# Kernel tuning notes

Measured on AMD Instinct MI355X. Metric: run time of the kernel, lower is better.

## Reference

```python
import jax, jax.numpy as jnp
import numpy as np

N = 32768
D = 512          # query_dim = key_dim = value_dim
H = 8            # num_heads


def setup_inputs() -> dict:
    key = jax.random.key(0)
    ks = jax.random.split(key, 8)
    s = 0.02
    return {
        "queries": jax.random.normal(ks[0], (N, D), dtype=jnp.float32),
        "keys": jax.random.normal(ks[1], (N, D), dtype=jnp.float32),
        "values": jax.random.normal(ks[2], (N, D), dtype=jnp.float32),
        # Linear weights stored as [in, out] (torch stores [out, in]; math identical)
        "Wq": jax.random.normal(ks[3], (D, D * H), dtype=jnp.float32) * s,
        "Wk": jax.random.normal(ks[4], (D, D * H), dtype=jnp.float32) * s,
        "Wv": jax.random.normal(ks[5], (D, D * H), dtype=jnp.float32) * s,
        "Wo": jax.random.normal(ks[6], (D * H, D), dtype=jnp.float32) * s,
        "bo": jax.random.normal(ks[7], (D,), dtype=jnp.float32) * s,
    }


def reference(queries, keys, values, Wq, Wk, Wv, Wo, bo):
    # Projections: [N, D] -> [N, H, D]
    Q = (queries @ Wq).reshape(-1, H, D)
    K = (keys @ Wk).reshape(-1, H, D)
    V = (values @ Wv).reshape(-1, H, D)
    # Per-token attention across the HEADS axis (faithful to torch.bmm on [N,H,D])
    attn = jnp.einsum("nhd,ngd->nhg", Q, K)      # [N, H, H], no 1/sqrt(d) scaling
    attn = jax.nn.softmax(attn, axis=-1)
    out = jnp.einsum("nhg,ngd->nhd", attn, V)    # [N, H, D]
    out = out.reshape(-1, H * D)
    return out @ Wo + bo                           # [N, D]
```

## Files before the change

kernel.cpp:

```cpp
#include <hip/hip_runtime.h>
#include <hip/hip_bf16.h>
#include <cstdint>


typedef unsigned short u16;
typedef unsigned int u32;
typedef __bf16 bf16x8 __attribute__((ext_vector_type(8)));
typedef float f32x4 __attribute__((ext_vector_type(4)));

#define DEVI __device__ __forceinline__

DEVI float b2f(u16 u) {
    union { u32 i; float f; } c; c.i = ((u32)u) << 16; return c.f;
}
DEVI u16 f2b(float f) {
    union { float f; u32 i; } c; c.f = f;
    return (u16)((c.i + 0x7FFFu + ((c.i >> 16) & 1u)) >> 16);
}

DEVI void async16(const u16* g, u16* l) {
    __builtin_amdgcn_global_load_lds(
        (const __attribute__((address_space(1))) u32*)g,
        (__attribute__((address_space(3))) u32*)l, 16, 0, 0);
}


__global__ __launch_bounds__(256) void cvt_bf16(const float* __restrict__ in,
                                                u16* __restrict__ out) {
    const int i = blockIdx.x * 256 + threadIdx.x;
    const float4 a = ((const float4*)in)[2 * i];
    const float4 b = ((const float4*)in)[2 * i + 1];
    union { u16 u[8]; uint4 v; } r;
    r.u[0] = f2b(a.x); r.u[1] = f2b(a.y); r.u[2] = f2b(a.z); r.u[3] = f2b(a.w);
    r.u[4] = f2b(b.x); r.u[5] = f2b(b.y); r.u[6] = f2b(b.z); r.u[7] = f2b(b.w);
    ((uint4*)out)[i] = r.v;
}

__global__ void transpose_cvt(const float* __restrict__ in, u16* __restrict__ out,
                              int R, int C) {
    __shared__ float tile[32][33];
    const int c0 = blockIdx.x * 32, r0 = blockIdx.y * 32;
    const int x = threadIdx.x, y = threadIdx.y;
#pragma unroll
    for (int i = 0; i < 4; ++i) {
        const int r = y + i * 8;
        tile[x][r] = in[(long)(r0 + r) * C + c0 + x];
    }
    __syncthreads();
#pragma unroll
    for (int i = 0; i < 4; ++i) {
        const int c = y + i * 8;
        out[(long)(c0 + c) * R + r0 + x] = f2b(tile[c][x]);
    }
}


template <int F32OUT>
__global__ __launch_bounds__(256) void gemm_bt(
    const u16* __restrict__ Ab, const u16* __restrict__ Bb,
    void* __restrict__ Cv, const float* __restrict__ bias,
    int M, int N, int K, long sAz, long sBz, long sCz) {
    __shared__ u16 As[2 * 4096];
    __shared__ u16 Bs[2 * 4096];
    const int tid = threadIdx.x;
    const int wave = tid >> 6, lane = tid & 63;
    const int z = blockIdx.z;
    const u16* A = Ab + (long)z * sAz;
    const u16* BT = Bb + (long)z * sBz;

    int bx, by;
    {
        const int b = blockIdx.y * gridDim.x + blockIdx.x;
        if ((gridDim.x & 7) == 0) {
            const int cb = gridDim.x >> 3;
            const int xcd = b & 7, j = b >> 3;
            bx = xcd * cb + (j % cb);
            by = j / cb;
        } else { bx = blockIdx.x; by = blockIdx.y; }
    }
    const long row0 = (long)by * 128, col0 = (long)bx * 128;
    const int wm = (wave >> 1) * 64, wn = (wave & 1) * 64;
    const int mrow = lane & 15, quad = lane >> 4;

    f32x4 acc[4][4] = {};

    const u16* pA = A + (row0 + wave * 32 + (lane >> 2)) * (long)K + (lane & 3) * 8;
    const u16* pB = BT + (col0 + wave * 32 + (lane >> 2)) * (long)K + (lane & 3) * 8;
    u16* lA = As + wave * 1024;
    u16* lB = Bs + wave * 1024;
    const long skip = 16 * (long)K;

    async16(pA, lA);
    async16(pA + skip, lA + 512);
    async16(pB, lB);
    async16(pB + skip, lB + 512);

    for (int k0 = 0; k0 < K; k0 += 32) {
        const int cur = (k0 >> 5) & 1;
        __syncthreads();
        if (k0 + 32 < K) {
            const int nb = (cur ^ 1) * 4096;
            const long o = k0 + 32;
            async16(pA + o, lA + nb);
            async16(pA + o + skip, lA + nb + 512);
            async16(pB + o, lB + nb);
            async16(pB + o + skip, lB + nb + 512);
        }
        const u16* sA = As + cur * 4096;
        const u16* sB = Bs + cur * 4096;
        bf16x8 af[4], bfr[4];
#pragma unroll
        for (int i = 0; i < 4; ++i)
            af[i] = *(const bf16x8*)(sA + (wm + i * 16 + mrow) * 32 + quad * 8);
#pragma unroll
        for (int j = 0; j < 4; ++j)
            bfr[j] = *(const bf16x8*)(sB + (wn + j * 16 + mrow) * 32 + quad * 8);
#pragma unroll
        for (int i = 0; i < 4; ++i)
#pragma unroll
            for (int j = 0; j < 4; ++j)
                acc[i][j] = __builtin_amdgcn_mfma_f32_16x16x32_bf16(
                    af[i], bfr[j], acc[i][j], 0, 0, 0);
    }

#pragma unroll
    for (int i = 0; i < 4; ++i) {
        const long r = row0 + wm + i * 16 + quad * 4;
#pragma unroll
        for (int j = 0; j < 4; ++j) {
            const long c = col0 + wn + j * 16 + mrow;
            if (F32OUT) {
                float* C = (float*)Cv + (long)z * sCz;
                const float bv = bias[c];
#pragma unroll
                for (int rr = 0; rr < 4; ++rr)
                    C[(r + rr) * (long)N + c] = acc[i][j][rr] + bv;
            } else {
                u16* C = (u16*)Cv + (long)z * sCz;
#pragma unroll
                for (int rr = 0; rr < 4; ++rr)
                    C[(r + rr) * (long)N + c] = f2b(acc[i][j][rr]);
            }
        }
    }
}


__global__ __launch_bounds__(256) void attn_kernel(
    const u16* __restrict__ Qg, const u16* __restrict__ Kg,
    const u16* __restrict__ Vg, u16* __restrict__ Og) {
    __shared__ uint4 sQ[512], sK[512], sV[512];
    __shared__ float part[4][64];
    __shared__ float logitS[64];
    __shared__ float probS[64];
    const int t = threadIdx.x;
    const long base = (long)blockIdx.x * 4096;

    const uint4* q4 = (const uint4*)(Qg + base);
    const uint4* k4 = (const uint4*)(Kg + base);
    const uint4* v4 = (const uint4*)(Vg + base);
    sQ[t] = q4[t]; sQ[t + 256] = q4[t + 256];
    sK[t] = k4[t]; sK[t + 256] = k4[t + 256];
    sV[t] = v4[t]; sV[t + 256] = v4[t + 256];
    __syncthreads();

    const u16* Qs = (const u16*)sQ;
    const u16* Ks = (const u16*)sK;
    const u16* Vs = (const u16*)sV;

    {
        const int pr = t & 63, ch = t >> 6;
        const int h = pr >> 3, g = pr & 7;
        const u16* qp = Qs + h * 512 + ch * 128;
        const u16* kp = Ks + g * 512 + ch * 128;
        float s = 0.f;
#pragma unroll
        for (int i = 0; i < 128; ++i) s += b2f(qp[i]) * b2f(kp[i]);
        part[ch][pr] = s;
    }
    __syncthreads();
    if (t < 64) logitS[t] = part[0][t] + part[1][t] + part[2][t] + part[3][t];
    __syncthreads();
    if (t < 8) {
        float m = logitS[t * 8];
#pragma unroll
        for (int g = 1; g < 8; ++g) m = fmaxf(m, logitS[t * 8 + g]);
        float e[8], sum = 0.f;
#pragma unroll
        for (int g = 0; g < 8; ++g) { e[g] = __expf(logitS[t * 8 + g] - m); sum += e[g]; }
        const float inv = 1.f / sum;
#pragma unroll
        for (int g = 0; g < 8; ++g) probS[t * 8 + g] = e[g] * inv;
    }
    __syncthreads();

    const int hh = t >> 5, d0 = (t & 31) * 16;
    float p[8];
#pragma unroll
    for (int g = 0; g < 8; ++g) p[g] = probS[hh * 8 + g];
    float o[16];
#pragma unroll
    for (int j = 0; j < 16; ++j) o[j] = 0.f;
#pragma unroll
    for (int g = 0; g < 8; ++g) {
        const u16* vp = Vs + g * 512 + d0;
#pragma unroll
        for (int j = 0; j < 16; ++j) o[j] += p[g] * b2f(vp[j]);
    }
    union { u16 u[16]; uint4 v[2]; } ob;
#pragma unroll
    for (int j = 0; j < 16; ++j) ob.u[j] = f2b(o[j]);
    uint4* op = (uint4*)(Og + base + hh * 512 + d0);
    op[0] = ob.v[0]; op[1] = ob.v[1];
}


extern "C" void kernel_launch(void* const* d_in, const int* in_sizes, int n_in,
                              void* d_out, int out_size, void* d_ws, size_t ws_size,
                              hipStream_t stream) {
    const float* Xq = (const float*)d_in[0];
    const float* Xk = (const float*)d_in[1];
    const float* Xv = (const float*)d_in[2];
    const float* Wq = (const float*)d_in[3];
    const float* Wk = (const float*)d_in[4];
    const float* Wv = (const float*)d_in[5];
    const float* Wo = (const float*)d_in[6];
    const float* bo = (const float*)d_in[7];

    const int N = 32768;
    const size_t FIXED = 16777216ull;
    int Mc = N;
    while (Mc > 128 && FIXED + (size_t)Mc * 27648ull > ws_size) Mc >>= 1;
    if (FIXED + (size_t)Mc * 27648ull > ws_size) return;

    char* ws = (char*)d_ws;
    u16* WqT = (u16*)(ws);
    u16* WoT = (u16*)(ws + 12582912ull);
    u16* Xqb = (u16*)(ws + FIXED);
    u16* Qc  = Xqb + (size_t)3 * Mc * 512;
    u16* Kc  = Qc + (size_t)Mc * 4096;
    u16* Vc  = Kc + (size_t)Mc * 4096;

    dim3 tb(32, 8);
    transpose_cvt<<<dim3(128, 16), tb, 0, stream>>>(Wq, WqT, 512, 4096);
    transpose_cvt<<<dim3(128, 16), tb, 0, stream>>>(Wk, WqT + 2097152, 512, 4096);
    transpose_cvt<<<dim3(128, 16), tb, 0, stream>>>(Wv, WqT + 4194304, 512, 4096);
    transpose_cvt<<<dim3(16, 128), tb, 0, stream>>>(Wo, WoT, 4096, 512);

    const dim3 gProj(4096 / 128, Mc / 128, 3);
    const dim3 gOut(512 / 128, Mc / 128, 1);
    for (int m0 = 0; m0 < N; m0 += Mc) {
        const long xoff = (long)m0 * 512;
        cvt_bf16<<<Mc / 4, 256, 0, stream>>>(Xq + xoff, Xqb);
        cvt_bf16<<<Mc / 4, 256, 0, stream>>>(Xk + xoff, Xqb + (size_t)Mc * 512);
        cvt_bf16<<<Mc / 4, 256, 0, stream>>>(Xv + xoff, Xqb + (size_t)2 * Mc * 512);
        gemm_bt<0><<<gProj, 256, 0, stream>>>(Xqb, WqT, Qc, nullptr,
                                              Mc, 4096, 512,
                                              (long)Mc * 512, 2097152L,
                                              (long)Mc * 4096);
        attn_kernel<<<Mc, 256, 0, stream>>>(Qc, Kc, Vc, Qc);
        gemm_bt<1><<<gOut, 256, 0, stream>>>(Qc, WoT, (float*)d_out + xoff, bo,
                                             Mc, 512, 4096, 0L, 0L, 0L);
    }
}
```

Baseline: 1.422 ms.

## Swizzle GEMM LDS layout, fuse input casts, run one full output GEMM

XOR-swizzles the 16-byte column groups in the GEMM's LDS tiles so fragment reads from different rows fall on different banks. The three input bf16 conversions are merged into one launch using blockIdx.z. When the workspace is large enough, attention output for all rows goes to a dedicated buffer and the output projection runs once over all N rows instead of per chunk. The chunk size is capped at 8192, and the buffer adds a 256MB workspace requirement, with the old per-chunk path kept as a fallback.

Measured after the change: 1.389 ms. 1.02x faster.

```diff
diff --git a/kernel.cpp b/kernel.cpp
--- a/kernel.cpp
+++ b/kernel.cpp
@@ -25,15 +25,18 @@
 }
 
 
-__global__ __launch_bounds__(256) void cvt_bf16(const float* __restrict__ in,
-                                                u16* __restrict__ out) {
+__global__ __launch_bounds__(256) void cvt3_bf16(
+    const float* __restrict__ a, const float* __restrict__ b,
+    const float* __restrict__ c, u16* __restrict__ out, long ostride) {
+    const float* in = (blockIdx.z == 0) ? a : (blockIdx.z == 1) ? b : c;
+    u16* o = out + (long)blockIdx.z * ostride;
     const int i = blockIdx.x * 256 + threadIdx.x;
-    const float4 a = ((const float4*)in)[2 * i];
-    const float4 b = ((const float4*)in)[2 * i + 1];
+    const float4 x = ((const float4*)in)[2 * i];
+    const float4 y = ((const float4*)in)[2 * i + 1];
     union { u16 u[8]; uint4 v; } r;
-    r.u[0] = f2b(a.x); r.u[1] = f2b(a.y); r.u[2] = f2b(a.z); r.u[3] = f2b(a.w);
-    r.u[4] = f2b(b.x); r.u[5] = f2b(b.y); r.u[6] = f2b(b.z); r.u[7] = f2b(b.w);
-    ((uint4*)out)[i] = r.v;
+    r.u[0] = f2b(x.x); r.u[1] = f2b(x.y); r.u[2] = f2b(x.z); r.u[3] = f2b(x.w);
+    r.u[4] = f2b(y.x); r.u[5] = f2b(y.y); r.u[6] = f2b(y.z); r.u[7] = f2b(y.w);
+    ((uint4*)o)[i] = r.v;
 }
 
 __global__ void transpose_cvt(const float* __restrict__ in, u16* __restrict__ out,
@@ -84,8 +87,10 @@
 
     f32x4 acc[4][4] = {};
 
-    const u16* pA = A + (row0 + wave * 32 + (lane >> 2)) * (long)K + (lane & 3) * 8;
-    const u16* pB = BT + (col0 + wave * 32 + (lane >> 2)) * (long)K + (lane & 3) * 8;
+    const int srow = lane >> 2;
+    const int sg = (lane & 3) ^ ((lane >> 3) & 3);
+    const u16* pA = A + (row0 + wave * 32 + srow) * (long)K + sg * 8;
+    const u16* pB = BT + (col0 + wave * 32 + srow) * (long)K + sg * 8;
     u16* lA = As + wave * 1024;
     u16* lB = Bs + wave * 1024;
     const long skip = 16 * (long)K;
@@ -95,6 +100,7 @@
     async16(pB, lB);
     async16(pB + skip, lB + 512);
 
+    const int cg = quad ^ ((mrow >> 1) & 3);
     for (int k0 = 0; k0 < K; k0 += 32) {
         const int cur = (k0 >> 5) & 1;
         __syncthreads();
@@ -111,10 +117,10 @@
         bf16x8 af[4], bfr[4];
 #pragma unroll
         for (int i = 0; i < 4; ++i)
-            af[i] = *(const bf16x8*)(sA + (wm + i * 16 + mrow) * 32 + quad * 8);
+            af[i] = *(const bf16x8*)(sA + (wm + i * 16 + mrow) * 32 + cg * 8);
 #pragma unroll
         for (int j = 0; j < 4; ++j)
-            bfr[j] = *(const bf16x8*)(sB + (wn + j * 16 + mrow) * 32 + quad * 8);
+            bfr[j] = *(const bf16x8*)(sB + (wn + j * 16 + mrow) * 32 + cg * 8);
 #pragma unroll
         for (int i = 0; i < 4; ++i)
 #pragma unroll
@@ -228,18 +234,16 @@
     const float* bo = (const float*)d_in[7];
 
     const int N = 32768;
-    const size_t FIXED = 16777216ull;
-    int Mc = N;
-    while (Mc > 128 && FIXED + (size_t)Mc * 27648ull > ws_size) Mc >>= 1;
-    if (FIXED + (size_t)Mc * 27648ull > ws_size) return;
+    const size_t W = 16777216ull;
+    const size_t AO = 268435456ull;
+
+    int McA = 0;
+    for (int m = 8192; m >= 1024; m >>= 1)
+        if (W + AO + (size_t)m * 27648ull <= ws_size) { McA = m; break; }
 
     char* ws = (char*)d_ws;
     u16* WqT = (u16*)(ws);
     u16* WoT = (u16*)(ws + 12582912ull);
-    u16* Xqb = (u16*)(ws + FIXED);
-    u16* Qc  = Xqb + (size_t)3 * Mc * 512;
-    u16* Kc  = Qc + (size_t)Mc * 4096;
-    u16* Vc  = Kc + (size_t)Mc * 4096;
 
     dim3 tb(32, 8);
     transpose_cvt<<<dim3(128, 16), tb, 0, stream>>>(Wq, WqT, 512, 4096);
@@ -247,19 +251,47 @@
     transpose_cvt<<<dim3(128, 16), tb, 0, stream>>>(Wv, WqT + 4194304, 512, 4096);
     transpose_cvt<<<dim3(16, 128), tb, 0, stream>>>(Wo, WoT, 4096, 512);
 
-    const dim3 gProj(4096 / 128, Mc / 128, 3);
-    const dim3 gOut(512 / 128, Mc / 128, 1);
-    for (int m0 = 0; m0 < N; m0 += Mc) {
-        const long xoff = (long)m0 * 512;
-        cvt_bf16<<<Mc / 4, 256, 0, stream>>>(Xq + xoff, Xqb);
-        cvt_bf16<<<Mc / 4, 256, 0, stream>>>(Xk + xoff, Xqb + (size_t)Mc * 512);
-        cvt_bf16<<<Mc / 4, 256, 0, stream>>>(Xv + xoff, Xqb + (size_t)2 * Mc * 512);
-        gemm_bt<0><<<gProj, 256, 0, stream>>>(Xqb, WqT, Qc, nullptr,
-                                              Mc, 4096, 512,
-                                              (long)Mc * 512, 2097152L,
-                                              (long)Mc * 4096);
-        attn_kernel<<<Mc, 256, 0, stream>>>(Qc, Kc, Vc, Qc);
-        gemm_bt<1><<<gOut, 256, 0, stream>>>(Qc, WoT, (float*)d_out + xoff, bo,
-                                             Mc, 512, 4096, 0L, 0L, 0L);
-    }
-}
+    if (McA) {
+        const int Mc = McA;
+        u16* Ao  = (u16*)(ws + W);
+        u16* Xb  = (u16*)(ws + W + AO);
+        u16* Qc  = Xb + (size_t)3 * Mc * 512;
+        u16* Kc  = Qc + (size_t)Mc * 4096;
+        u16* Vc  = Kc + (size_t)Mc * 4096;
+        const dim3 gProj(32, Mc / 128, 3);
+        for (int m0 = 0; m0 < N; m0 += Mc) {
+            const long xoff = (long)m0 * 512;
+            cvt3_bf16<<<dim3(Mc / 4, 1, 3), 256, 0, stream>>>(
+                Xq + xoff, Xk + xoff, Xv + xoff, Xb, (long)Mc * 512);
+            gemm_bt<0><<<gProj, 256, 0, stream>>>(Xb, WqT, Qc, nullptr,
+                                                  Mc, 4096, 512,
+                                                  (long)Mc * 512, 2097152L,
+                                                  (long)Mc * 4096);
+            attn_kernel<<<Mc, 256, 0, stream>>>(Qc, Kc, Vc, Ao + (long)m0 * 4096);
+        }
+        gemm_bt<1><<<dim3(4, 256, 1), 256, 0, stream>>>(
+            Ao, WoT, d_out, bo, N, 512, 4096, 0L, 0L, 0L);
+    } else {
+        int Mc = 8192;
+        while (Mc > 128 && W + (size_t)Mc * 27648ull > ws_size) Mc >>= 1;
+        if (W + (size_t)Mc * 27648ull > ws_size) return;
+        u16* Xb = (u16*)(ws + W);
+        u16* Qc = Xb + (size_t)3 * Mc * 512;
+        u16* Kc = Qc + (size_t)Mc * 4096;
+        u16* Vc = Kc + (size_t)Mc * 4096;
+        const dim3 gProj(32, Mc / 128, 3);
+        const dim3 gOut(4, Mc / 128, 1);
+        for (int m0 = 0; m0 < N; m0 += Mc) {
+            const long xoff = (long)m0 * 512;
+            cvt3_bf16<<<dim3(Mc / 4, 1, 3), 256, 0, stream>>>(
+                Xq + xoff, Xk + xoff, Xv + xoff, Xb, (long)Mc * 512);
+            gemm_bt<0><<<gProj, 256, 0, stream>>>(Xb, WqT, Qc, nullptr,
+                                                  Mc, 4096, 512,
+                                                  (long)Mc * 512, 2097152L,
+                                                  (long)Mc * 4096);
+            attn_kernel<<<Mc, 256, 0, stream>>>(Qc, Kc, Vc, Qc);
+            gemm_bt<1><<<gOut, 256, 0, stream>>>(Qc, WoT, (float*)d_out + xoff, bo,
+                                                 Mc, 512, 4096, 0L, 0L, 0L);
+        }
+    }
+}
```
